# Optimization experiments

Measured on AMD Instinct MI355X. Metric: run time of the kernel, lower is better.

## Reference

```python
import jax, jax.numpy as jnp
import numpy as np

B, L, D = 4, 4096, 8
K_MAX = 64


def _pack_codes(x):
    # binary_quantize (x > 0) then pack the d sign bits into one int32 code.
    bits = (x > 0).astype(jnp.int32)                       # [B, L, d]
    powers = 2 ** jnp.arange(x.shape[-1], dtype=jnp.int32)  # [d]
    return jnp.einsum('bld,d->bl', bits, powers)           # [B, L]


def setup_inputs() -> dict:
    key = jax.random.key(0)
    kq, kk = jax.random.split(key)
    return {
        'query_up': jax.random.normal(kq, (B, L, D), dtype=jnp.float32),
        'key_up': jax.random.normal(kk, (B, L, D), dtype=jnp.float32),
        'head_idx': 0,
    }


def reference(query_up, key_up, head_idx):
    # Wu-Manber matches the first prefix_len sign bits; the Trie matches the
    # full sign-bit vector, so their set intersection is exactly the set of
    # keys whose full binary signature equals the query's.
    Lq = query_up.shape[1]
    q_codes = _pack_codes(query_up)   # [B, L]
    k_codes = _pack_codes(key_up)     # [B, L]
    match = q_codes[:, :, None] == k_codes[:, None, :]     # [B, L, L] bool
    # score = key index j if it matches, else L (sentinel); smallest K_MAX
    # scores = first K_MAX matching key indices in ascending order.
    idx = jnp.arange(Lq, dtype=jnp.int32)
    score = jnp.where(match, idx[None, None, :], jnp.int32(Lq))  # [B, L, L]
    neg_top, _ = jax.lax.top_k(-score, K_MAX)              # [B, L, K_MAX]
    cand = -neg_top                                        # ascending matches, then L pads
    cand = jnp.where(cand < Lq, cand, -1)                  # pad with -1 like torch.full
    # merge_candidate_indices_groups: cat (single group) -> sort -> take k_max.
    # torch.sort puts the -1 padding first; unique_consecutive over full
    # [B, L] slices is an identity here (no two whole slices coincide).
    return jnp.sort(cand, axis=-1).astype(jnp.int64)       # [B, L, K_MAX]
```

## Files before the change

### kernel.cpp

```cpp
#include <hip/hip_runtime.h>

#define BB      4
#define LL      4096
#define DD      8
#define KMAX    64
#define NCODES  256

__global__ void pack_key_codes(const float* __restrict__ key_up,
                               int* __restrict__ k_codes) {
    int idx = blockIdx.x * blockDim.x + threadIdx.x;
    if (idx >= BB * LL) return;
    const float4* p = reinterpret_cast<const float4*>(key_up + (size_t)idx * DD);
    float4 a = p[0];
    float4 b = p[1];
    int code = ((int)(a.x > 0.f))
             | ((int)(a.y > 0.f) << 1)
             | ((int)(a.z > 0.f) << 2)
             | ((int)(a.w > 0.f) << 3)
             | ((int)(b.x > 0.f) << 4)
             | ((int)(b.y > 0.f) << 5)
             | ((int)(b.z > 0.f) << 6)
             | ((int)(b.w > 0.f) << 7);
    k_codes[idx] = code;
}

__global__ void build_res(const int* __restrict__ k_codes,
                          int* __restrict__ res) {
    __shared__ int buf[4][KMAX];
    const int wslot = threadIdx.x >> 6;
    const int lane  = threadIdx.x & 63;
    const int wid   = blockIdx.x * 4 + wslot;
    const int b     = wid >> 8;
    const int c     = wid & (NCODES - 1);
    const int* codes = k_codes + b * LL;

    int found = 0;
    for (int base = 0; base < LL; base += 64) {
        if (found >= KMAX) break;
        int j = base + lane;
        bool m = (codes[j] == c);
        unsigned long long mask = __ballot(m);
        if (m) {
            int rank = found + (int)__popcll(mask & ((1ull << lane) - 1ull));
            if (rank < KMAX) buf[wslot][rank] = j;
        }
        found += (int)__popcll(mask);
    }
    int mcount = found < KMAX ? found : KMAX;
    int pad    = KMAX - mcount;
    int val    = (lane < pad) ? -1 : buf[wslot][lane - pad];
    res[((size_t)b * NCODES + c) * KMAX + lane] = val;
}

__global__ void gather_out(const float* __restrict__ query_up,
                           const int* __restrict__ res,
                           int* __restrict__ out) {
    int tid  = blockIdx.x * blockDim.x + threadIdx.x;
    int q    = tid >> 6;
    int lane = threadIdx.x & 63;
    if (q >= BB * LL) return;
    int b = q >> 12;
    float x = query_up[(size_t)q * DD + (lane & 7)];
    unsigned long long mask = __ballot(x > 0.f);
    int code = (int)(mask & 0xffull);
    out[tid] = res[((size_t)b * NCODES + code) * KMAX + lane];
}

extern "C" void kernel_launch(void* const* d_in, const int* in_sizes, int n_in,
                              void* d_out, int out_size, void* d_ws, size_t ws_size,
                              hipStream_t stream) {
    const float* query_up = (const float*)d_in[0];
    const float* key_up   = (const float*)d_in[1];

    int* out     = (int*)d_out;
    int* k_codes = (int*)d_ws;
    int* res     = (int*)((char*)d_ws + (size_t)BB * LL * sizeof(int));

    pack_key_codes<<<(BB * LL + 255) / 256, 256, 0, stream>>>(key_up, k_codes);
    build_res<<<(BB * NCODES) / 4, 256, 0, stream>>>(k_codes, res);
    gather_out<<<(BB * LL * KMAX) / 256, 256, 0, stream>>>(query_up, res, out);
}
```

Measured before the change: 79.21 us.

## Fuse key packing into table build and vectorize candidate gather

Key-code packing moves into the table-building kernel. Each of 64 blocks of 1024 threads packs one batch's 4096 codes into shared memory, and each wave scans them from registers to collect up to 64 matching indices. This removes one kernel launch and the global round-trip for the key codes. The cost is that every block recomputes the codes for its batch, and the early exit once 64 matches are found is gone. The gather kernel now serves four queries per wave with int4 loads and stores, cutting thread count and memory instructions by four.

Measured after the change: 65.51 us. 1.21x faster.

```diff
diff --git a/kernel.cpp b/kernel.cpp
--- a/kernel.cpp
+++ b/kernel.cpp
@@ -6,49 +6,56 @@
 #define KMAX    64
 #define NCODES  256
 
-__global__ void pack_key_codes(const float* __restrict__ key_up,
-                               int* __restrict__ k_codes) {
-    int idx = blockIdx.x * blockDim.x + threadIdx.x;
-    if (idx >= BB * LL) return;
-    const float4* p = reinterpret_cast<const float4*>(key_up + (size_t)idx * DD);
-    float4 a = p[0];
-    float4 b = p[1];
-    int code = ((int)(a.x > 0.f))
-             | ((int)(a.y > 0.f) << 1)
-             | ((int)(a.z > 0.f) << 2)
-             | ((int)(a.w > 0.f) << 3)
-             | ((int)(b.x > 0.f) << 4)
-             | ((int)(b.y > 0.f) << 5)
-             | ((int)(b.z > 0.f) << 6)
-             | ((int)(b.w > 0.f) << 7);
-    k_codes[idx] = code;
-}
+__global__ void __launch_bounds__(1024)
+build_res(const float* __restrict__ key_up, int* __restrict__ res) {
+    __shared__ int scodes[LL];
+    __shared__ int sbuf[16][KMAX];
 
-__global__ void build_res(const int* __restrict__ k_codes,
-                          int* __restrict__ res) {
-    __shared__ int buf[4][KMAX];
-    const int wslot = threadIdx.x >> 6;
-    const int lane  = threadIdx.x & 63;
-    const int wid   = blockIdx.x * 4 + wslot;
-    const int b     = wid >> 8;
-    const int c     = wid & (NCODES - 1);
-    const int* codes = k_codes + b * LL;
+    const int b = blockIdx.x >> 4;
+    const int g = blockIdx.x & 15;
+    const int t = threadIdx.x;
 
+    const float4* kp = reinterpret_cast<const float4*>(key_up + (size_t)b * LL * DD);
+#pragma unroll
+    for (int j = 0; j < 4; ++j) {
+        int k = t + j * 1024;
+        float4 a = kp[k * 2];
+        float4 c4 = kp[k * 2 + 1];
+        int code = ((int)(a.x > 0.f))
+                 | ((int)(a.y > 0.f) << 1)
+                 | ((int)(a.z > 0.f) << 2)
+                 | ((int)(a.w > 0.f) << 3)
+                 | ((int)(c4.x > 0.f) << 4)
+                 | ((int)(c4.y > 0.f) << 5)
+                 | ((int)(c4.z > 0.f) << 6)
+                 | ((int)(c4.w > 0.f) << 7);
+        scodes[k] = code;
+    }
+    __syncthreads();
+
+    const int w    = t >> 6;
+    const int lane = t & 63;
+    const int c    = g * 16 + w;
+
+    int v[64];
+#pragma unroll
+    for (int i = 0; i < 64; ++i) v[i] = scodes[i * 64 + lane];
+
+    const unsigned long long prefix = (1ull << lane) - 1ull;
     int found = 0;
-    for (int base = 0; base < LL; base += 64) {
-        if (found >= KMAX) break;
-        int j = base + lane;
-        bool m = (codes[j] == c);
+#pragma unroll
+    for (int i = 0; i < 64; ++i) {
+        bool m = (v[i] == c);
         unsigned long long mask = __ballot(m);
         if (m) {
-            int rank = found + (int)__popcll(mask & ((1ull << lane) - 1ull));
-            if (rank < KMAX) buf[wslot][rank] = j;
+            int rank = found + (int)__popcll(mask & prefix);
+            if (rank < KMAX) sbuf[w][rank] = i * 64 + lane;
         }
         found += (int)__popcll(mask);
     }
     int mcount = found < KMAX ? found : KMAX;
     int pad    = KMAX - mcount;
-    int val    = (lane < pad) ? -1 : buf[wslot][lane - pad];
+    int val    = (lane < pad) ? -1 : sbuf[w][lane - pad];
     res[((size_t)b * NCODES + c) * KMAX + lane] = val;
 }
 
@@ -56,14 +63,16 @@
                            const int* __restrict__ res,
                            int* __restrict__ out) {
     int tid  = blockIdx.x * blockDim.x + threadIdx.x;
-    int q    = tid >> 6;
     int lane = threadIdx.x & 63;
-    if (q >= BB * LL) return;
-    int b = q >> 12;
-    float x = query_up[(size_t)q * DD + (lane & 7)];
+    int wq   = tid >> 6;
+    int myq  = wq * 4 + (lane >> 4);
+    int b    = myq >> 12;
+    float x  = query_up[(size_t)myq * DD + (lane & 7)];
     unsigned long long mask = __ballot(x > 0.f);
-    int code = (int)(mask & 0xffull);
-    out[tid] = res[((size_t)b * NCODES + code) * KMAX + lane];
+    int code = (int)((mask >> ((lane >> 4) << 4)) & 0xffull);
+    const int4* src = reinterpret_cast<const int4*>(res + ((size_t)b * NCODES + code) * KMAX);
+    int4 vv = src[lane & 15];
+    reinterpret_cast<int4*>(out)[(size_t)myq * 16 + (lane & 15)] = vv;
 }
 
 extern "C" void kernel_launch(void* const* d_in, const int* in_sizes, int n_in,
@@ -72,11 +81,9 @@
     const float* query_up = (const float*)d_in[0];
     const float* key_up   = (const float*)d_in[1];
 
-    int* out     = (int*)d_out;
-    int* k_codes = (int*)d_ws;
-    int* res     = (int*)((char*)d_ws + (size_t)BB * LL * sizeof(int));
+    int* out = (int*)d_out;
+    int* res = (int*)d_ws;
 
-    pack_key_codes<<<(BB * LL + 255) / 256, 256, 0, stream>>>(key_up, k_codes);
-    build_res<<<(BB * NCODES) / 4, 256, 0, stream>>>(k_codes, res);
-    gather_out<<<(BB * LL * KMAX) / 256, 256, 0, stream>>>(query_up, res, out);
+    build_res<<<BB * 16, 1024, 0, stream>>>(key_up, res);
+    gather_out<<<(BB * LL * 16) / 256, 256, 0, stream>>>(query_up, res, out);
 }
```
